# Optimization experiments

Hardware: AMD Instinct MI355X
Metric: run time of the kernel (lower is better)

The kernel has to match this reference:

```python
import jax, jax.numpy as jnp
import numpy as np

N = 50000      # nodes per graph
E = 1_600_000  # edges per graph (before self-loops)
D = 128        # node feature dim
H = 9          # attention heads
C = 8          # channels per head
HC = H * C     # 72
NEG_SLOPE = 0.2


def setup_inputs() -> dict:
    key = jax.random.key(0)
    ks = iter(jax.random.split(key, 32))
    inp = {}
    for i in (1, 2, 3):
        inp[f"x{i}"] = jax.random.normal(next(ks), (N, D), dtype=jnp.float32)
        inp[f"edge_index{i}"] = jax.random.randint(next(ks), (2, E), 0, N, dtype=jnp.int64)
        inp[f"W{i}"] = jax.random.normal(next(ks), (D, HC), dtype=jnp.float32) * (1.0 / np.sqrt(D))
        inp[f"att_src{i}"] = jax.random.normal(next(ks), (H, C), dtype=jnp.float32) * 0.1
        inp[f"att_dst{i}"] = jax.random.normal(next(ks), (H, C), dtype=jnp.float32) * 0.1
        inp[f"b{i}"] = jnp.zeros((HC,), dtype=jnp.float32)
    inp["fnn_W"] = jax.random.normal(next(ks), (3 * HC, 2), dtype=jnp.float32) * (1.0 / np.sqrt(3 * HC))
    inp["fnn_b"] = jnp.zeros((2,), dtype=jnp.float32)
    return inp


def gat_conv(x, edge_index, W, att_src, att_dst, bias):
    """PyG GATConv (eval mode): linear -> per-edge LeakyReLU score -> edge softmax
    over incoming edges per dst node -> scatter-add aggregate. Self-loops added."""
    n = x.shape[0]
    loop = jnp.arange(n, dtype=edge_index.dtype)
    src = jnp.concatenate([edge_index[0], loop])  # [E+N]
    dst = jnp.concatenate([edge_index[1], loop])
    h = (x @ W).reshape(n, H, C)                  # [N,H,C]
    a_s = jnp.einsum('nhc,hc->nh', h, att_src)    # [N,H]
    a_d = jnp.einsum('nhc,hc->nh', h, att_dst)
    alpha = jax.nn.leaky_relu(a_s[src] + a_d[dst], NEG_SLOPE)   # [E+N,H]
    m = jax.ops.segment_max(alpha, dst, num_segments=n)         # stable softmax per dst
    alpha = jnp.exp(alpha - m[dst])
    denom = jax.ops.segment_sum(alpha, dst, num_segments=n)
    alpha = alpha / (denom[dst] + 1e-16)
    out = jax.ops.segment_sum(h[src] * alpha[:, :, None], dst, num_segments=n)
    return out.reshape(n, HC) + bias


def reference(x1, x2, x3, edge_index1, edge_index2, edge_index3,
              W1, att_src1, att_dst1, b1,
              W2, att_src2, att_dst2, b2,
              W3, att_src3, att_dst3, b3,
              fnn_W, fnn_b):
    o1 = gat_conv(x1, edge_index1, W1, att_src1, att_dst1, b1)
    o2 = gat_conv(x2, edge_index2, W2, att_src2, att_dst2, b2)
    o3 = gat_conv(x3, edge_index3, W3, att_src3, att_dst3, b3)
    x = jax.nn.relu(jnp.concatenate([o1, o2, o3], axis=1))  # [N, 216]
    logits = x @ fnn_W + fnn_b                              # [N, 2]
    return jax.nn.softmax(logits, axis=1)
```

## Files before the change

### kernel.cpp

```cpp
#include <hip/hip_runtime.h>
#include <hip/hip_fp16.h>

#define NN 50000
#define NE 1600000
#define DD 128
#define NH 9
#define NC 8
#define HCH 72
#define NEG 0.2f
#define NBUCK 196
#define NSEG 16
#define SPAD 17
#define EPB 8
#define BCH (256*EPB)
#define BSTRIDE 10240
#define GEMMB 586
#define BINB ((NE + BCH - 1) / BCH)

__device__ __forceinline__ unsigned short f2h(float f) {
  return __half_as_ushort(__float2half_rn(f));
}
__device__ __forceinline__ float h2f(unsigned short u) {
  return __half2float(__ushort_as_half(u));
}
__device__ __forceinline__ float hlo(unsigned u) {
  return __half2float(__ushort_as_half((unsigned short)(u & 0xFFFFu)));
}
__device__ __forceinline__ float hhi(unsigned u) {
  return __half2float(__ushort_as_half((unsigned short)(u >> 16)));
}

struct GP {
  const float* x; const int* ei; const float* W;
  const float* as; const float* ad; const float* b;
  uint4* h2;
  unsigned short* as2;
  float* a_d; float* out;
  int* offs2;
  int* bcursor;
  unsigned int* pairs;
  int* csr;
};
struct GT { GP g[3]; };

__global__ __launch_bounds__(256) void k_gemm_bin(GT t) {
  const GP G = t.g[blockIdx.z];
  __shared__ float Wl[DD * HCH];
  const int tid = threadIdx.x;

  if (blockIdx.x >= GEMMB) {
    int* lh    = (int*)Wl;
    int* lbase = lh + 256;
    int* lcur  = lbase + 256;
    const int e0 = (blockIdx.x - GEMMB) * BCH;
    for (int i = tid; i < NBUCK; i += 256) lh[i] = 0;
    __syncthreads();
    int dsts[EPB], srcs[EPB];
    #pragma unroll
    for (int k = 0; k < EPB; ++k) {
      const int e = e0 + k * 256 + tid;
      if (e < NE) {
        dsts[k] = G.ei[NE + e];
        srcs[k] = G.ei[e];
        atomicAdd(&lh[dsts[k] >> 8], 1);
      } else dsts[k] = -1;
    }
    __syncthreads();
    for (int i = tid; i < NBUCK; i += 256) {
      int c = lh[i];
      lbase[i] = c ? atomicAdd(&G.bcursor[i], c) : 0;
      lcur[i] = 0;
    }
    __syncthreads();
    #pragma unroll
    for (int k = 0; k < EPB; ++k) {
      if (dsts[k] >= 0) {
        int b = dsts[k] >> 8;
        int pos = lbase[b] + atomicAdd(&lcur[b], 1);
        if (pos < BSTRIDE)
          G.pairs[(size_t)b * BSTRIDE + pos] =
              (unsigned)srcs[k] | ((unsigned)(dsts[k] & 255) << 16);
      }
    }
    return;
  }

  {
    const float4* Wg = (const float4*)G.W;
    float4* Wd = (float4*)Wl;
    #pragma unroll
    for (int i = 0; i < 9; ++i) Wd[tid + 256 * i] = Wg[tid + 256 * i];
  }
  const int gid = blockIdx.x * 256 + tid;
  __syncthreads();
  if (gid >= NN * 3) return;
  const int n  = gid / 3;
  const int g3 = gid - n * 3;
  float4 acc[6];
  #pragma unroll
  for (int i = 0; i < 6; ++i) acc[i] = make_float4(0.f, 0.f, 0.f, 0.f);
  const float4* x4 = (const float4*)(G.x + (size_t)n * DD);
  const float* wb = Wl + g3 * 24;

  for (int k4 = 0; k4 < DD / 4; ++k4) {
    const float4 xv = x4[k4];
    #pragma unroll
    for (int kk = 0; kk < 4; ++kk) {
      const float xk = (kk == 0) ? xv.x : (kk == 1) ? xv.y : (kk == 2) ? xv.z : xv.w;
      const float4* wr = (const float4*)(wb + (k4 * 4 + kk) * HCH);
      #pragma unroll
      for (int c = 0; c < 6; ++c) {
        float4 wv = wr[c];
        acc[c].x = fmaf(xk, wv.x, acc[c].x);
        acc[c].y = fmaf(xk, wv.y, acc[c].y);
        acc[c].z = fmaf(xk, wv.z, acc[c].z);
        acc[c].w = fmaf(xk, wv.w, acc[c].w);
      }
    }
  }

  #pragma unroll
  for (int j = 0; j < 3; ++j) {
    const int hd = 3 * g3 + j;
    const float4 a0 = acc[2 * j];
    const float4 a1 = acc[2 * j + 1];
    const float4 As0 = *(const float4*)(G.as + hd * NC);
    const float4 As1 = *(const float4*)(G.as + hd * NC + 4);
    const float4 Ad0 = *(const float4*)(G.ad + hd * NC);
    const float4 Ad1 = *(const float4*)(G.ad + hd * NC + 4);
    float ssrc = a0.x*As0.x + a0.y*As0.y + a0.z*As0.z + a0.w*As0.w
               + a1.x*As1.x + a1.y*As1.y + a1.z*As1.z + a1.w*As1.w;
    float sdst = a0.x*Ad0.x + a0.y*Ad0.y + a0.z*Ad0.z + a0.w*Ad0.w
               + a1.x*Ad1.x + a1.y*Ad1.y + a1.z*Ad1.z + a1.w*Ad1.w;
    G.as2[n * NH + hd] = f2h(ssrc);
    G.a_d[n * NH + hd] = sdst;
    uint4 hv;
    hv.x = (unsigned)f2h(a0.x) | ((unsigned)f2h(a0.y) << 16);
    hv.y = (unsigned)f2h(a0.z) | ((unsigned)f2h(a0.w) << 16);
    hv.z = (unsigned)f2h(a1.x) | ((unsigned)f2h(a1.y) << 16);
    hv.w = (unsigned)f2h(a1.z) | ((unsigned)f2h(a1.w) << 16);
    G.h2[(size_t)n * NH + hd] = hv;
  }
}

__global__ __launch_bounds__(256) void k_scat2(GT t) {
  const GP G = t.g[blockIdx.z];
  const int b = blockIdx.x;
  const int d0 = b << 8;
  __shared__ int cnt[256 * SPAD];
  __shared__ int ssum[256];
  const int tid = threadIdx.x;
  const int estart = b * BSTRIDE;
  const int eend = estart + G.bcursor[b];
  for (int i = tid; i < 256 * SPAD; i += 256) cnt[i] = 0;
  __syncthreads();
  for (int e = estart + tid; e < eend; e += 256) {
    unsigned p = G.pairs[e];
    int key = (int)((p >> 16) * SPAD + ((p & 0xFFFFu) >> 12));
    atomicAdd(&cnt[key], 1);
  }
  __syncthreads();
  int local[NSEG];
  int sum = 0;
  #pragma unroll
  for (int i = 0; i < NSEG; ++i) { local[i] = sum; sum += cnt[tid * SPAD + i]; }
  ssum[tid] = sum;
  __syncthreads();
  int run = sum;
  for (int off = 1; off < 256; off <<= 1) {
    int u = (tid >= off) ? ssum[tid - off] : 0;
    __syncthreads();
    run += u;
    ssum[tid] = run;
    __syncthreads();
  }
  const int texcl = run - sum;
  int* o2 = G.offs2 + ((size_t)d0 << 4);
  #pragma unroll
  for (int i = 0; i < NSEG; ++i) {
    int v = estart + texcl + local[i];
    cnt[tid * SPAD + i] = v;
    o2[tid * NSEG + i] = v;
  }
  __syncthreads();
  for (int e = estart + tid; e < eend; e += 256) {
    unsigned p = G.pairs[e];
    int key = (int)((p >> 16) * SPAD + ((p & 0xFFFFu) >> 12));
    int pos = atomicAdd(&cnt[key], 1);
    G.csr[pos] = (int)(p & 0xFFFFu);
  }
}

__global__ __launch_bounds__(256) void k_agg(GP G) {
  const int gid = blockIdx.x * 256 + threadIdx.x;
  const bool active = (gid < NN * NH);
  int n = 0, head = 0;
  if (active) { n = gid / NH; head = gid - n * NH; }
  float denom = 0.f;
  float4 acc0 = make_float4(0.f, 0.f, 0.f, 0.f);
  float4 acc1 = make_float4(0.f, 0.f, 0.f, 0.f);
  float ad_n = 0.f;
  int gb[5] = {0, 0, 0, 0, 0};
  if (active) {
    ad_n = G.a_d[n * NH + head];
    const int* o2 = G.offs2 + ((size_t)n << 4);
    gb[0] = o2[0]; gb[1] = o2[4]; gb[2] = o2[8]; gb[3] = o2[12]; gb[4] = o2[13];
    float sl = h2f(G.as2[n * NH + head]) + ad_n;
    sl = (sl > 0.f) ? sl : NEG * sl;
    float wl = __expf(sl);
    uint4 hs = G.h2[(size_t)n * NH + head];
    denom = wl;
    acc0.x = wl * hlo(hs.x); acc0.y = wl * hhi(hs.x);
    acc0.z = wl * hlo(hs.y); acc0.w = wl * hhi(hs.y);
    acc1.x = wl * hlo(hs.z); acc1.y = wl * hhi(hs.z);
    acc1.z = wl * hlo(hs.w); acc1.w = wl * hhi(hs.w);
  }
  #pragma unroll
  for (int g = 0; g < 4; ++g) {
    int e = gb[g];
    const int en = gb[g + 1];
    for (; e + 4 <= en; e += 4) {
      int s0 = G.csr[e];
      int s1 = G.csr[e + 1];
      int s2 = G.csr[e + 2];
      int s3 = G.csr[e + 3];
      unsigned short u0 = G.as2[s0 * NH + head];
      unsigned short u1 = G.as2[s1 * NH + head];
      unsigned short u2 = G.as2[s2 * NH + head];
      unsigned short u3 = G.as2[s3 * NH + head];
      uint4 v0 = G.h2[(size_t)s0 * NH + head];
      uint4 v1 = G.h2[(size_t)s1 * NH + head];
      uint4 v2 = G.h2[(size_t)s2 * NH + head];
      uint4 v3 = G.h2[(size_t)s3 * NH + head];
      float t0 = h2f(u0) + ad_n;
      float t1 = h2f(u1) + ad_n;
      float t2 = h2f(u2) + ad_n;
      float t3 = h2f(u3) + ad_n;
      t0 = (t0 > 0.f) ? t0 : NEG * t0;
      t1 = (t1 > 0.f) ? t1 : NEG * t1;
      t2 = (t2 > 0.f) ? t2 : NEG * t2;
      t3 = (t3 > 0.f) ? t3 : NEG * t3;
      float w0 = __expf(t0);
      float w1 = __expf(t1);
      float w2 = __expf(t2);
      float w3 = __expf(t3);
      denom += (w0 + w1) + (w2 + w3);
      acc0.x = fmaf(w0, hlo(v0.x), acc0.x); acc0.y = fmaf(w0, hhi(v0.x), acc0.y);
      acc0.z = fmaf(w0, hlo(v0.y), acc0.z); acc0.w = fmaf(w0, hhi(v0.y), acc0.w);
      acc1.x = fmaf(w0, hlo(v0.z), acc1.x); acc1.y = fmaf(w0, hhi(v0.z), acc1.y);
      acc1.z = fmaf(w0, hlo(v0.w), acc1.z); acc1.w = fmaf(w0, hhi(v0.w), acc1.w);
      acc0.x = fmaf(w1, hlo(v1.x), acc0.x); acc0.y = fmaf(w1, hhi(v1.x), acc0.y);
      acc0.z = fmaf(w1, hlo(v1.y), acc0.z); acc0.w = fmaf(w1, hhi(v1.y), acc0.w);
      acc1.x = fmaf(w1, hlo(v1.z), acc1.x); acc1.y = fmaf(w1, hhi(v1.z), acc1.y);
      acc1.z = fmaf(w1, hlo(v1.w), acc1.z); acc1.w = fmaf(w1, hhi(v1.w), acc1.w);
      acc0.x = fmaf(w2, hlo(v2.x), acc0.x); acc0.y = fmaf(w2, hhi(v2.x), acc0.y);
      acc0.z = fmaf(w2, hlo(v2.y), acc0.z); acc0.w = fmaf(w2, hhi(v2.y), acc0.w);
      acc1.x = fmaf(w2, hlo(v2.z), acc1.x); acc1.y = fmaf(w2, hhi(v2.z), acc1.y);
      acc1.z = fmaf(w2, hlo(v2.w), acc1.z); acc1.w = fmaf(w2, hhi(v2.w), acc1.w);
      acc0.x = fmaf(w3, hlo(v3.x), acc0.x); acc0.y = fmaf(w3, hhi(v3.x), acc0.y);
      acc0.z = fmaf(w3, hlo(v3.y), acc0.z); acc0.w = fmaf(w3, hhi(v3.y), acc0.w);
      acc1.x = fmaf(w3, hlo(v3.z), acc1.x); acc1.y = fmaf(w3, hhi(v3.z), acc1.y);
      acc1.z = fmaf(w3, hlo(v3.w), acc1.z); acc1.w = fmaf(w3, hhi(v3.w), acc1.w);
    }
    for (; e < en; ++e) {
      int src = G.csr[e];
      float sc = h2f(G.as2[src * NH + head]) + ad_n;
      sc = (sc > 0.f) ? sc : NEG * sc;
      float w = __expf(sc);
      uint4 hv = G.h2[(size_t)src * NH + head];
      denom += w;
      acc0.x = fmaf(w, hlo(hv.x), acc0.x); acc0.y = fmaf(w, hhi(hv.x), acc0.y);
      acc0.z = fmaf(w, hlo(hv.y), acc0.z); acc0.w = fmaf(w, hhi(hv.y), acc0.w);
      acc1.x = fmaf(w, hlo(hv.z), acc1.x); acc1.y = fmaf(w, hhi(hv.z), acc1.y);
      acc1.z = fmaf(w, hlo(hv.w), acc1.z); acc1.w = fmaf(w, hhi(hv.w), acc1.w);
    }
    __syncthreads();
  }
  if (!active) return;
  float inv = 1.f / (denom + 1e-16f);
  const float* bp = G.b + head * NC;
  float4 o0, o1;
  o0.x = acc0.x * inv + bp[0]; o0.y = acc0.y * inv + bp[1];
  o0.z = acc0.z * inv + bp[2]; o0.w = acc0.w * inv + bp[3];
  o1.x = acc1.x * inv + bp[4]; o1.y = acc1.y * inv + bp[5];
  o1.z = acc1.z * inv + bp[6]; o1.w = acc1.w * inv + bp[7];
  float4* op = (float4*)(G.out + (size_t)n * HCH + head * NC);
  op[0] = o0; op[1] = o1;
}

__global__ __launch_bounds__(256) void k_fnn(const float* __restrict__ o1,
                                             const float* __restrict__ o2,
                                             const float* __restrict__ o3,
                                             const float* __restrict__ fw,
                                             const float* __restrict__ fb,
                                             float* __restrict__ out) {
  const int tid = blockIdx.x * 256 + threadIdx.x;
  const int n = tid >> 6;
  const int lane = tid & 63;
  if (n >= NN) return;
  float acc0 = 0.f, acc1 = 0.f;
  for (int j = lane; j < 3 * HCH; j += 64) {
    const int g = j / HCH;
    const int c = j - g * HCH;
    const float* og = (g == 0) ? o1 : (g == 1) ? o2 : o3;
    float v = og[(size_t)n * HCH + c];
    v = v > 0.f ? v : 0.f;
    acc0 = fmaf(v, fw[2 * j], acc0);
    acc1 = fmaf(v, fw[2 * j + 1], acc1);
  }
  #pragma unroll
  for (int off = 32; off > 0; off >>= 1) {
    acc0 += __shfl_down(acc0, off, 64);
    acc1 += __shfl_down(acc1, off, 64);
  }
  if (lane == 0) {
    float l0 = acc0 + fb[0], l1 = acc1 + fb[1];
    float m = fmaxf(l0, l1);
    float e0 = __expf(l0 - m), e1 = __expf(l1 - m);
    float inv = 1.f / (e0 + e1);
    out[(size_t)n * 2] = e0 * inv;
    out[(size_t)n * 2 + 1] = e1 * inv;
  }
}

extern "C" void kernel_launch(void* const* d_in, const int* in_sizes, int n_in,
                              void* d_out, int out_size, void* d_ws, size_t ws_size,
                              hipStream_t stream) {
  (void)in_sizes; (void)n_in; (void)out_size; (void)ws_size;
  GT t;
  char* w = (char*)d_ws;
  size_t off = 0;
  auto carve = [&](size_t bytes) -> void* {
    void* p = w + off;
    off = (off + bytes + 255) & ~(size_t)255;
    return p;
  };
  int* bc_all = (int*)carve(3 * 256 * 4);
  for (int g = 0; g < 3; ++g) {
    GP& G = t.g[g];
    G.x  = (const float*)d_in[6 * g + 0];
    G.ei = (const int*)d_in[6 * g + 1];
    G.W  = (const float*)d_in[6 * g + 2];
    G.as = (const float*)d_in[6 * g + 3];
    G.ad = (const float*)d_in[6 * g + 4];
    G.b  = (const float*)d_in[6 * g + 5];
    G.bcursor = bc_all + g * 256;
    G.h2   = (uint4*)carve((size_t)NN * NH * 16);
    G.as2  = (unsigned short*)carve((size_t)NN * NH * 2);
    G.a_d  = (float*)carve((size_t)NN * NH * 4);
    G.out  = (float*)carve((size_t)NN * HCH * 4);
    G.offs2 = (int*)carve((size_t)NBUCK * 256 * NSEG * 4);
    G.pairs = (unsigned int*)carve((size_t)NBUCK * BSTRIDE * 4);
    G.csr   = (int*)carve((size_t)NBUCK * BSTRIDE * 4);
  }
  const float* fw = (const float*)d_in[18];
  const float* fb = (const float*)d_in[19];
  float* outp = (float*)d_out;

  dim3 b256(256, 1, 1);
  hipMemsetAsync(bc_all, 0, 3 * 256 * 4, stream);
  k_gemm_bin<<<dim3(GEMMB + BINB, 1, 3), b256, 0, stream>>>(t);
  k_scat2   <<<dim3(NBUCK, 1, 3), b256, 0, stream>>>(t);
  for (int g = 0; g < 3; ++g)
    k_agg   <<<dim3((NN * NH + 255) / 256, 1, 1), b256, 0, stream>>>(t.g[g]);
  k_fnn     <<<(NN * 64 + 255) / 256, b256, 0, stream>>>(t.g[0].out, t.g[1].out, t.g[2].out, fw, fb, outp);
}
```

Measured before the change: 437.8 us.

## Compute node projection with split-fp16 MFMA instead of scalar FP32 FMAs

Replaces the per-thread scalar FP32 x@W loop with MFMA 16x16x32 f16 matrix instructions. Each block handles 64 nodes, and W is stored transposed in LDS as fp16. x is split into hi and lo fp16 parts to keep accuracy. Results are staged through LDS as fp16 before the attention-score dot products and stores. This cuts the ALU cost of the GEMM stage and changes block count and LDS use. The risk is lower precision from rounding W to fp16, and the attention scores are now computed from fp16-rounded h.

```diff
diff --git a/kernel.cpp b/kernel.cpp
--- a/kernel.cpp
+++ b/kernel.cpp
@@ -14,8 +14,13 @@
 #define EPB 8
 #define BCH (256*EPB)
 #define BSTRIDE 10240
-#define GEMMB 586
+#define GEMMB2 ((NN + 63) / 64)
 #define BINB ((NE + BCH - 1) / BCH)
+#define WTP 136
+#define CLP 88
+
+typedef _Float16 f16x8 __attribute__((ext_vector_type(8)));
+typedef float f32x4 __attribute__((ext_vector_type(4)));
 
 __device__ __forceinline__ unsigned short f2h(float f) {
   return __half_as_ushort(__float2half_rn(f));
@@ -45,14 +50,14 @@
 
 __global__ __launch_bounds__(256) void k_gemm_bin(GT t) {
   const GP G = t.g[blockIdx.z];
-  __shared__ float Wl[DD * HCH];
+  __shared__ __align__(16) char smem[80 * WTP * 2 + 64 * CLP * 2];
   const int tid = threadIdx.x;
 
-  if (blockIdx.x >= GEMMB) {
-    int* lh    = (int*)Wl;
+  if (blockIdx.x >= GEMMB2) {
+    int* lh    = (int*)smem;
     int* lbase = lh + 256;
     int* lcur  = lbase + 256;
-    const int e0 = (blockIdx.x - GEMMB) * BCH;
+    const int e0 = (blockIdx.x - GEMMB2) * BCH;
     for (int i = tid; i < NBUCK; i += 256) lh[i] = 0;
     __syncthreads();
     int dsts[EPB], srcs[EPB];
@@ -85,61 +90,78 @@
     return;
   }
 
-  {
-    const float4* Wg = (const float4*)G.W;
-    float4* Wd = (float4*)Wl;
-    #pragma unroll
-    for (int i = 0; i < 9; ++i) Wd[tid + 256 * i] = Wg[tid + 256 * i];
-  }
-  const int gid = blockIdx.x * 256 + tid;
-  __syncthreads();
-  if (gid >= NN * 3) return;
-  const int n  = gid / 3;
-  const int g3 = gid - n * 3;
-  float4 acc[6];
-  #pragma unroll
-  for (int i = 0; i < 6; ++i) acc[i] = make_float4(0.f, 0.f, 0.f, 0.f);
-  const float4* x4 = (const float4*)(G.x + (size_t)n * DD);
-  const float* wb = Wl + g3 * 24;
-
-  for (int k4 = 0; k4 < DD / 4; ++k4) {
-    const float4 xv = x4[k4];
-    #pragma unroll
-    for (int kk = 0; kk < 4; ++kk) {
-      const float xk = (kk == 0) ? xv.x : (kk == 1) ? xv.y : (kk == 2) ? xv.z : xv.w;
-      const float4* wr = (const float4*)(wb + (k4 * 4 + kk) * HCH);
-      #pragma unroll
-      for (int c = 0; c < 6; ++c) {
-        float4 wv = wr[c];
-        acc[c].x = fmaf(xk, wv.x, acc[c].x);
-        acc[c].y = fmaf(xk, wv.y, acc[c].y);
-        acc[c].z = fmaf(xk, wv.z, acc[c].z);
-        acc[c].w = fmaf(xk, wv.w, acc[c].w);
-      }
-    }
-  }
-
-  #pragma unroll
-  for (int j = 0; j < 3; ++j) {
-    const int hd = 3 * g3 + j;
-    const float4 a0 = acc[2 * j];
-    const float4 a1 = acc[2 * j + 1];
+  _Float16* Wt = (_Float16*)smem;
+  _Float16* Cl = (_Float16*)(smem + 80 * WTP * 2);
+
+  for (int i = tid; i < DD * 80; i += 256) {
+    const int k = i / 80;
+    const int c = i - k * 80;
+    const float v = (c < HCH) ? G.W[k * HCH + c] : 0.f;
+    Wt[c * WTP + k] = (_Float16)v;
+  }
+  __syncthreads();
+
+  const int wv = tid >> 6;
+  const int ln = tid & 63;
+  const int rl = ln & 15;
+  const int kg = ln >> 4;
+  const int n0 = blockIdx.x << 6;
+  int arow = n0 + wv * 16 + rl;
+  if (arow >= NN) arow = NN - 1;
+  const float4* xr = (const float4*)(G.x + (size_t)arow * DD) + (kg << 1);
+
+  f32x4 acc[5];
+  #pragma unroll
+  for (int ct = 0; ct < 5; ++ct) acc[ct] = (f32x4){0.f, 0.f, 0.f, 0.f};
+
+  #pragma unroll
+  for (int ks = 0; ks < 4; ++ks) {
+    const float4 xa = xr[ks * 8];
+    const float4 xb = xr[ks * 8 + 1];
+    float xs[8] = {xa.x, xa.y, xa.z, xa.w, xb.x, xb.y, xb.z, xb.w};
+    f16x8 ahi, alo;
+    #pragma unroll
+    for (int j = 0; j < 8; ++j) {
+      const _Float16 h = (_Float16)xs[j];
+      ahi[j] = h;
+      alo[j] = (_Float16)(xs[j] - (float)h);
+    }
+    const int kb = ks * 32 + kg * 8;
+    #pragma unroll
+    for (int ct = 0; ct < 5; ++ct) {
+      const f16x8 bf = *(const f16x8*)&Wt[(ct * 16 + rl) * WTP + kb];
+      acc[ct] = __builtin_amdgcn_mfma_f32_16x16x32_f16(ahi, bf, acc[ct], 0, 0, 0);
+      acc[ct] = __builtin_amdgcn_mfma_f32_16x16x32_f16(alo, bf, acc[ct], 0, 0, 0);
+    }
+  }
+
+  #pragma unroll
+  for (int ct = 0; ct < 5; ++ct) {
+    #pragma unroll
+    for (int j = 0; j < 4; ++j)
+      Cl[(wv * 16 + kg * 4 + j) * CLP + ct * 16 + rl] = (_Float16)acc[ct][j];
+  }
+  __syncthreads();
+
+  for (int p = tid; p < 64 * NH; p += 256) {
+    const int node = p / NH;
+    const int hd = p - node * NH;
+    const int n = n0 + node;
+    if (n >= NN) continue;
+    const uint4 hv = *(const uint4*)&Cl[node * CLP + hd * NC];
+    const float h0 = hlo(hv.x), h1 = hhi(hv.x), h2v = hlo(hv.y), h3 = hhi(hv.y);
+    const float h4 = hlo(hv.z), h5 = hhi(hv.z), h6 = hlo(hv.w), h7 = hhi(hv.w);
     const float4 As0 = *(const float4*)(G.as + hd * NC);
     const float4 As1 = *(const float4*)(G.as + hd * NC + 4);
     const float4 Ad0 = *(const float4*)(G.ad + hd * NC);
     const float4 Ad1 = *(const float4*)(G.ad + hd * NC + 4);
-    float ssrc = a0.x*As0.x + a0.y*As0.y + a0.z*As0.z + a0.w*As0.w
-               + a1.x*As1.x + a1.y*As1.y + a1.z*As1.z + a1.w*As1.w;
-    float sdst = a0.x*Ad0.x + a0.y*Ad0.y + a0.z*Ad0.z + a0.w*Ad0.w
-               + a1.x*Ad1.x + a1.y*Ad1.y + a1.z*Ad1.z + a1.w*Ad1.w;
+    const float ssrc = h0 * As0.x + h1 * As0.y + h2v * As0.z + h3 * As0.w
+                     + h4 * As1.x + h5 * As1.y + h6 * As1.z + h7 * As1.w;
+    const float sdst = h0 * Ad0.x + h1 * Ad0.y + h2v * Ad0.z + h3 * Ad0.w
+                     + h4 * Ad1.x + h5 * Ad1.y + h6 * Ad1.z + h7 * Ad1.w;
+    G.h2[(size_t)n * NH + hd] = hv;
     G.as2[n * NH + hd] = f2h(ssrc);
     G.a_d[n * NH + hd] = sdst;
-    uint4 hv;
-    hv.x = (unsigned)f2h(a0.x) | ((unsigned)f2h(a0.y) << 16);
-    hv.y = (unsigned)f2h(a0.z) | ((unsigned)f2h(a0.w) << 16);
-    hv.z = (unsigned)f2h(a1.x) | ((unsigned)f2h(a1.y) << 16);
-    hv.w = (unsigned)f2h(a1.z) | ((unsigned)f2h(a1.w) << 16);
-    G.h2[(size_t)n * NH + hd] = hv;
   }
 }
 
@@ -359,7 +381,7 @@
 
   dim3 b256(256, 1, 1);
   hipMemsetAsync(bc_all, 0, 3 * 256 * 4, stream);
-  k_gemm_bin<<<dim3(GEMMB + BINB, 1, 3), b256, 0, stream>>>(t);
+  k_gemm_bin<<<dim3(GEMMB2 + BINB, 1, 3), b256, 0, stream>>>(t);
   k_scat2   <<<dim3(NBUCK, 1, 3), b256, 0, stream>>>(t);
   for (int g = 0; g < 3; ++g)
     k_agg   <<<dim3((NN * NH + 255) / 256, 1, 1), b256, 0, stream>>>(t.g[g]);
```

After: 433.2 us. About the same (-1.0%).
